# Kernel optimization log

Hardware: AMD Instinct MI355X
Metric: run time of the kernel (lower is better)

Reference implementation:

```python
import jax, jax.numpy as jnp
import numpy as np

B, N, K = 4096, 10000, 100

def setup_inputs() -> dict:
    key = jax.random.key(0)
    k1, k2 = jax.random.split(key)
    nodes = jax.random.uniform(k1, (B, N, 2), dtype=jnp.float32)
    candidate_indices = jax.random.randint(k2, (B, K), 0, N, dtype=jnp.int64)
    return {"nodes": nodes, "candidate_indices": candidate_indices}

def reference(nodes, candidate_indices):
    # nodes: [B, N, 2], candidate_indices: [B, K] with -1 = padding
    valid = candidate_indices != -1                      # [B, K]
    safe_idx = jnp.where(valid, candidate_indices, 0)    # [B, K]
    # gather candidate coords: [B, K, 2]
    cand = jnp.take_along_axis(
        nodes, jnp.broadcast_to(safe_idx[:, :, None], safe_idx.shape + (2,)), axis=1)
    big = jnp.asarray(jnp.inf, nodes.dtype)
    x = cand[:, :, 0]
    y = cand[:, :, 1]
    x_min = jnp.min(jnp.where(valid, x,  big), axis=1)   # [B]
    x_max = jnp.max(jnp.where(valid, x, -big), axis=1)
    y_min = jnp.min(jnp.where(valid, y,  big), axis=1)
    y_max = jnp.max(jnp.where(valid, y, -big), axis=1)
    span = jnp.maximum(x_max - x_min, y_max - y_min)
    r = 1.0 / jnp.clip(span, 1e-6)                       # [B]
    mins = jnp.stack([x_min, y_min], axis=-1)            # [B, 2]
    normalized = jnp.clip(r[:, None, None] * (nodes - mins[:, None, :]), 0.0, 1.0)
    any_valid = jnp.any(valid, axis=1)                   # [B]
    return jnp.where(any_valid[:, None, None], normalized, nodes)
```

## Files before the change

kernel.cpp:

```cpp
#include <hip/hip_runtime.h>
#include <math.h>

#define BATCH 4096
#define NNODES 10000
#define KCAND 100

__global__ void bbox_reduce_kernel(const float* __restrict__ nodes,
                                   const int* __restrict__ cand,
                                   float4* __restrict__ params) {
    const int wave = threadIdx.x >> 6;
    const int lane = threadIdx.x & 63;
    const int b = blockIdx.x * 4 + wave;
    if (b >= BATCH) return;

    const int* ib = cand + (size_t)b * KCAND;
    const float* nb = nodes + (size_t)b * (size_t)NNODES * 2;

    float xmin =  INFINITY, xmax = -INFINITY;
    float ymin =  INFINITY, ymax = -INFINITY;
    bool any = false;

    for (int c = lane; c < KCAND; c += 64) {
        int id = ib[c];
        if (id != -1) {
            any = true;
            const float2 p = *reinterpret_cast<const float2*>(nb + (size_t)id * 2);
            xmin = fminf(xmin, p.x);
            xmax = fmaxf(xmax, p.x);
            ymin = fminf(ymin, p.y);
            ymax = fmaxf(ymax, p.y);
        }
    }

    #pragma unroll
    for (int off = 32; off > 0; off >>= 1) {
        xmin = fminf(xmin, __shfl_xor(xmin, off, 64));
        xmax = fmaxf(xmax, __shfl_xor(xmax, off, 64));
        ymin = fminf(ymin, __shfl_xor(ymin, off, 64));
        ymax = fmaxf(ymax, __shfl_xor(ymax, off, 64));
    }
    const bool any_valid = __any(any);

    if (lane == 0) {
        float span = fmaxf(xmax - xmin, ymax - ymin);
        float r = 1.0f / fmaxf(span, 1e-6f);
        params[b] = make_float4(r, xmin, ymin, any_valid ? 1.0f : 0.0f);
    }
}

#define F4_PER_BATCH (NNODES * 2 / 4)

__global__ void normalize_kernel(const float* __restrict__ nodes,
                                 const float4* __restrict__ params,
                                 float* __restrict__ out) {
    const int b = blockIdx.y;
    const int i = blockIdx.x * blockDim.x + threadIdx.x;
    if (i >= F4_PER_BATCH) return;

    const float4 p = params[b];
    const float4* src = reinterpret_cast<const float4*>(nodes + (size_t)b * (NNODES * 2));
    float4* dst = reinterpret_cast<float4*>(out + (size_t)b * (NNODES * 2));

    float4 v = src[i];
    if (p.w != 0.0f) {
        v.x = fminf(fmaxf(p.x * (v.x - p.y), 0.0f), 1.0f);
        v.y = fminf(fmaxf(p.x * (v.y - p.z), 0.0f), 1.0f);
        v.z = fminf(fmaxf(p.x * (v.z - p.y), 0.0f), 1.0f);
        v.w = fminf(fmaxf(p.x * (v.w - p.z), 0.0f), 1.0f);
    }
    dst[i] = v;
}

extern "C" void kernel_launch(void* const* d_in, const int* in_sizes, int n_in,
                              void* d_out, int out_size, void* d_ws, size_t ws_size,
                              hipStream_t stream) {
    const float* nodes = (const float*)d_in[0];
    const int* cand = (const int*)d_in[1];
    float* out = (float*)d_out;
    float4* params = (float4*)d_ws;

    bbox_reduce_kernel<<<dim3(BATCH / 4), dim3(256), 0, stream>>>(nodes, cand, params);

    dim3 grid((F4_PER_BATCH + 255) / 256, BATCH);
    normalize_kernel<<<grid, dim3(256), 0, stream>>>(nodes, params, out);
}
```

Measured before the change: 126.0 us.

## Fuse bbox reduction and normalization into one per-batch kernel with nontemporal streaming

Merges the bbox reduction and normalize kernels into one kernel with one block per batch. Each block gathers the candidates, reduces across its waves through shared memory, then streams the batch's nodes using nontemporal loads and stores. This removes the second launch and the params workspace round trip. In exchange, each block now waits on the candidate gather latency before streaming, and the grid is coarser.

```diff
diff --git a/kernel.cpp b/kernel.cpp
--- a/kernel.cpp
+++ b/kernel.cpp
@@ -4,31 +4,32 @@
 #define BATCH 4096
 #define NNODES 10000
 #define KCAND 100
+#define F4_PER_BATCH (NNODES * 2 / 4)
 
-__global__ void bbox_reduce_kernel(const float* __restrict__ nodes,
-                                   const int* __restrict__ cand,
-                                   float4* __restrict__ params) {
-    const int wave = threadIdx.x >> 6;
-    const int lane = threadIdx.x & 63;
-    const int b = blockIdx.x * 4 + wave;
-    if (b >= BATCH) return;
+typedef float f4 __attribute__((ext_vector_type(4)));
 
-    const int* ib = cand + (size_t)b * KCAND;
-    const float* nb = nodes + (size_t)b * (size_t)NNODES * 2;
+__global__ __launch_bounds__(256) void fused_normalize_kernel(
+        const float* __restrict__ nodes,
+        const int* __restrict__ cand,
+        float* __restrict__ out) {
+    const int b = blockIdx.x;
+    const int tid = threadIdx.x;
+    const int wave = tid >> 6;
+    const int lane = tid & 63;
+
+    const float* nb = nodes + (size_t)b * (NNODES * 2);
 
     float xmin =  INFINITY, xmax = -INFINITY;
     float ymin =  INFINITY, ymax = -INFINITY;
-    bool any = false;
+    float any = 0.0f;
 
-    for (int c = lane; c < KCAND; c += 64) {
-        int id = ib[c];
+    if (tid < KCAND) {
+        int id = cand[(size_t)b * KCAND + tid];
         if (id != -1) {
-            any = true;
+            any = 1.0f;
             const float2 p = *reinterpret_cast<const float2*>(nb + (size_t)id * 2);
-            xmin = fminf(xmin, p.x);
-            xmax = fmaxf(xmax, p.x);
-            ymin = fminf(ymin, p.y);
-            ymax = fmaxf(ymax, p.y);
+            xmin = p.x; xmax = p.x;
+            ymin = p.y; ymax = p.y;
         }
     }
 
@@ -38,37 +39,45 @@
         xmax = fmaxf(xmax, __shfl_xor(xmax, off, 64));
         ymin = fminf(ymin, __shfl_xor(ymin, off, 64));
         ymax = fmaxf(ymax, __shfl_xor(ymax, off, 64));
+        any  = fmaxf(any,  __shfl_xor(any,  off, 64));
     }
-    const bool any_valid = __any(any);
 
+    __shared__ float sxmin[4], sxmax[4], symin[4], symax[4], sany[4];
     if (lane == 0) {
-        float span = fmaxf(xmax - xmin, ymax - ymin);
-        float r = 1.0f / fmaxf(span, 1e-6f);
-        params[b] = make_float4(r, xmin, ymin, any_valid ? 1.0f : 0.0f);
+        sxmin[wave] = xmin; sxmax[wave] = xmax;
+        symin[wave] = ymin; symax[wave] = ymax;
+        sany[wave]  = any;
     }
-}
+    __syncthreads();
 
-#define F4_PER_BATCH (NNODES * 2 / 4)
+    xmin = fminf(fminf(sxmin[0], sxmin[1]), fminf(sxmin[2], sxmin[3]));
+    xmax = fmaxf(fmaxf(sxmax[0], sxmax[1]), fmaxf(sxmax[2], sxmax[3]));
+    ymin = fminf(fminf(symin[0], symin[1]), fminf(symin[2], symin[3]));
+    ymax = fmaxf(fmaxf(symax[0], symax[1]), fmaxf(symax[2], symax[3]));
+    any  = fmaxf(fmaxf(sany[0],  sany[1]),  fmaxf(sany[2],  sany[3]));
 
-__global__ void normalize_kernel(const float* __restrict__ nodes,
-                                 const float4* __restrict__ params,
-                                 float* __restrict__ out) {
-    const int b = blockIdx.y;
-    const int i = blockIdx.x * blockDim.x + threadIdx.x;
-    if (i >= F4_PER_BATCH) return;
+    const float span = fmaxf(xmax - xmin, ymax - ymin);
+    const float r = 1.0f / fmaxf(span, 1e-6f);
+    const bool valid = (any != 0.0f);
 
-    const float4 p = params[b];
-    const float4* src = reinterpret_cast<const float4*>(nodes + (size_t)b * (NNODES * 2));
-    float4* dst = reinterpret_cast<float4*>(out + (size_t)b * (NNODES * 2));
+    const f4* src = reinterpret_cast<const f4*>(nb);
+    f4* dst = reinterpret_cast<f4*>(out + (size_t)b * (NNODES * 2));
 
-    float4 v = src[i];
-    if (p.w != 0.0f) {
-        v.x = fminf(fmaxf(p.x * (v.x - p.y), 0.0f), 1.0f);
-        v.y = fminf(fmaxf(p.x * (v.y - p.z), 0.0f), 1.0f);
-        v.z = fminf(fmaxf(p.x * (v.z - p.y), 0.0f), 1.0f);
-        v.w = fminf(fmaxf(p.x * (v.w - p.z), 0.0f), 1.0f);
+    if (valid) {
+        for (int i = tid; i < F4_PER_BATCH; i += 256) {
+            f4 v = __builtin_nontemporal_load(src + i);
+            v.x = fminf(fmaxf(r * (v.x - xmin), 0.0f), 1.0f);
+            v.y = fminf(fmaxf(r * (v.y - ymin), 0.0f), 1.0f);
+            v.z = fminf(fmaxf(r * (v.z - xmin), 0.0f), 1.0f);
+            v.w = fminf(fmaxf(r * (v.w - ymin), 0.0f), 1.0f);
+            __builtin_nontemporal_store(v, dst + i);
+        }
+    } else {
+        for (int i = tid; i < F4_PER_BATCH; i += 256) {
+            f4 v = __builtin_nontemporal_load(src + i);
+            __builtin_nontemporal_store(v, dst + i);
+        }
     }
-    dst[i] = v;
 }
 
 extern "C" void kernel_launch(void* const* d_in, const int* in_sizes, int n_in,
@@ -77,10 +86,6 @@
     const float* nodes = (const float*)d_in[0];
     const int* cand = (const int*)d_in[1];
     float* out = (float*)d_out;
-    float4* params = (float4*)d_ws;
 
-    bbox_reduce_kernel<<<dim3(BATCH / 4), dim3(256), 0, stream>>>(nodes, cand, params);
-
-    dim3 grid((F4_PER_BATCH + 255) / 256, BATCH);
-    normalize_kernel<<<grid, dim3(256), 0, stream>>>(nodes, params, out);
+    fused_normalize_kernel<<<dim3(BATCH), dim3(256), 0, stream>>>(nodes, cand, out);
 }
```

Result: no change. 127.2 us (+0.9%).
